# Kernel tuning notes

Hardware: AMD Instinct MI355X
Metric: run time of the kernel (lower is better)

## Reference

```python
import jax, jax.numpy as jnp
import numpy as np

L, E, H, C, N = 3, 512, 8, 64, 65536
DH = E // H
LN_EPS = 1e-5


def setup_inputs() -> dict:
    key = jax.random.key(0)
    ks = jax.random.split(key, 10)
    s = 1.0 / np.sqrt(E)
    return {
        "support_features": jax.random.normal(ks[0], (N, E), jnp.float32),
        "support_labels": jax.random.randint(ks[1], (N,), 0, C),
        "W1": jax.random.normal(ks[2], (L, E, E), jnp.float32) * s,
        "b1": jnp.zeros((L, E), jnp.float32),
        "gamma": jnp.ones((L, E), jnp.float32),
        "beta": jnp.zeros((L, E), jnp.float32),
        "W2": jax.random.normal(ks[3], (L, E, E), jnp.float32) * s,
        "b2": jnp.zeros((L, E), jnp.float32),
        "Wq": jax.random.normal(ks[4], (E, E), jnp.float32) * s,
        "bq": jnp.zeros((E,), jnp.float32),
        "Wk": jax.random.normal(ks[5], (E, E), jnp.float32) * s,
        "bk": jnp.zeros((E,), jnp.float32),
        "Wv": jax.random.normal(ks[6], (E, E), jnp.float32) * s,
        "bv": jnp.zeros((E,), jnp.float32),
        "Wo": jax.random.normal(ks[7], (E, E), jnp.float32) * s,
        "bo": jnp.zeros((E,), jnp.float32),
        "level_weights": jnp.ones((L,), jnp.float32) / L,
        "level_temps": jnp.ones((L,), jnp.float32),
    }


def _layer_norm(x, g, b):
    mu = jnp.mean(x, axis=-1, keepdims=True)
    var = jnp.var(x, axis=-1, keepdims=True)
    return (x - mu) * jax.lax.rsqrt(var + LN_EPS) * g + b


def reference(support_features, support_labels, W1, b1, gamma, beta, W2, b2,
              Wq, bq, Wk, bk, Wv, bv, Wo, bo, level_weights, level_temps):
    # class membership mask [C, N]; segment counts [C]
    onehot = support_labels[None, :] == jnp.arange(C)[:, None]
    counts = jnp.sum(onehot, axis=1).astype(support_features.dtype)
    scale = 1.0 / np.sqrt(DH)
    protos = []
    for l in range(L):  # small fixed number of levels
        # prototype MLP (dropout inactive at eval)
        h = jnp.maximum(_layer_norm(support_features @ W1[l] + b1[l], gamma[l], beta[l]), 0.0)
        feat = h @ W2[l] + b2[l]                              # [N, E]
        # per-class mean context (segment mean) -> query
        ctx = (onehot.astype(feat.dtype) @ feat) / counts[:, None]  # [C, E]
        q = (ctx @ Wq + bq).reshape(C, H, DH)
        k = (feat @ Wk + bk).reshape(N, H, DH)
        v = (feat @ Wv + bv).reshape(N, H, DH)
        scores = jnp.einsum('chd,nhd->chn', q, k) * scale      # [C, H, N]
        scores = jnp.where(onehot[:, None, :], scores, -jnp.inf)
        attn = jax.nn.softmax(scores, axis=-1)
        out = jnp.einsum('chn,nhd->chd', attn, v).reshape(C, E)
        protos.append(out @ Wo + bo)                           # [C, E]
    lw = jax.nn.softmax(level_weights)
    final = protos[0] * (lw[0] / level_temps[0])
    for i in range(1, L):
        final = final + protos[i] * (lw[i] / level_temps[i])
    return final
```

## Files before the change

### kernel.cpp

```cpp
#include <hip/hip_runtime.h>
#include <math.h>

#define N_SUP 65536
#define E_DIM 512
#define H_HEADS 8
#define C_CLS 64
#define DHD 64
#define L_LEV 3
#define LN_EPS 1e-5f
#define ATTN_SPLITS 8
#define CTX_SPLITS 16
#define SCAT_BLOCKS 256
#define KV_LD 1024

typedef _Float16 f16x8 __attribute__((ext_vector_type(8)));
typedef _Float16 f16x4 __attribute__((ext_vector_type(4)));
typedef float f32x4 __attribute__((ext_vector_type(4)));

__device__ __forceinline__ void gload_lds16(const void* g, void* lds) {
    __builtin_amdgcn_global_load_lds((const __attribute__((address_space(1))) void*)g,
                                     (__attribute__((address_space(3))) void*)lds,
                                     16, 0, 0);
}

__global__ __launch_bounds__(256)
void hgemm_bt(const _Float16* __restrict__ A, int lda, size_t aStride,
              const _Float16* __restrict__ Bt, size_t btStride,
              const float* __restrict__ bias, size_t biasStride,
              _Float16* __restrict__ C, int ldc, size_t cStride, int nCol) {
    const int z = blockIdx.y;
    A += z * aStride; Bt += z * btStride; bias += z * biasStride; C += z * cStride;

    const int nRow = gridDim.x / nCol;
    const int R = nRow < 64 ? nRow : 64;
    const int bid = blockIdx.x;
    const int bandSz = R * nCol;
    const int band = bid / bandSz;
    const int rem = bid % bandSz;
    const int colT = rem / R;
    const int rowT = band * R + (rem % R);

    __shared__ _Float16 As[128][32];
    __shared__ _Float16 Bs[128][32];
    const int tid = threadIdx.x;
    const int wave = tid >> 6, lane = tid & 63;
    const int row0 = rowT * 128, col0 = colT * 128;
    const int wm = (wave & 1) * 64, wn = (wave >> 1) * 64;

    const int ci0 = wave * 128 + lane, ci1 = ci0 + 64;
    const int r0 = ci0 >> 2, gc0 = (ci0 & 3) ^ ((r0 >> 1) & 3);
    const int r1 = ci1 >> 2, gc1 = (ci1 & 3) ^ ((r1 >> 1) & 3);
    const _Float16* Ar0 = A + (size_t)(row0 + r0) * lda + gc0 * 8;
    const _Float16* Ar1 = A + (size_t)(row0 + r1) * lda + gc1 * 8;
    const _Float16* Br0 = Bt + (size_t)(col0 + r0) * E_DIM + gc0 * 8;
    const _Float16* Br1 = Bt + (size_t)(col0 + r1) * E_DIM + gc1 * 8;
    char* ldsA = (char*)&As[0][0] + wave * 2048;
    char* ldsB = (char*)&Bs[0][0] + wave * 2048;

    const int m = lane & 15, q = lane >> 4;
    const int koff = ((q ^ ((m >> 1) & 3))) * 8;

    f32x4 acc[4][4];
#pragma unroll
    for (int i = 0; i < 4; ++i)
#pragma unroll
        for (int j = 0; j < 4; ++j) acc[i][j] = (f32x4){0.f, 0.f, 0.f, 0.f};

    for (int k0 = 0; k0 < E_DIM; k0 += 32) {
        gload_lds16(Ar0 + k0, ldsA);
        gload_lds16(Ar1 + k0, ldsA + 1024);
        gload_lds16(Br0 + k0, ldsB);
        gload_lds16(Br1 + k0, ldsB + 1024);
        __syncthreads();

        f16x8 af[4], bf[4];
#pragma unroll
        for (int i = 0; i < 4; ++i)
            af[i] = *(const f16x8*)&As[wm + i * 16 + m][koff];
#pragma unroll
        for (int j = 0; j < 4; ++j)
            bf[j] = *(const f16x8*)&Bs[wn + j * 16 + m][koff];
#pragma unroll
        for (int i = 0; i < 4; ++i)
#pragma unroll
            for (int j = 0; j < 4; ++j)
                acc[i][j] = __builtin_amdgcn_mfma_f32_16x16x32_f16(af[i], bf[j], acc[i][j], 0, 0, 0);
        __syncthreads();
    }

#pragma unroll
    for (int i = 0; i < 4; ++i) {
        const int rbase = row0 + wm + i * 16 + q * 4;
#pragma unroll
        for (int j = 0; j < 4; ++j) {
            const int col = col0 + wn + j * 16 + m;
            const float bv = bias[col];
#pragma unroll
            for (int r = 0; r < 4; ++r)
                C[(size_t)(rbase + r) * ldc + col] = (_Float16)(acc[i][j][r] + bv);
        }
    }
}

__global__ __launch_bounds__(256)
void conv32to16(const float* __restrict__ in, _Float16* __restrict__ out, int n4) {
    int i = blockIdx.x * 256 + threadIdx.x;
    if (i < n4) {
        f32x4 v = ((const f32x4*)in)[i];
        f16x4 o = {(_Float16)v[0], (_Float16)v[1], (_Float16)v[2], (_Float16)v[3]};
        ((f16x4*)out)[i] = o;
    }
}

__global__ __launch_bounds__(256)
void transpose_all(const float* __restrict__ W1, const float* __restrict__ Wk,
                   const float* __restrict__ Wv, const float* __restrict__ Wq,
                   _Float16* __restrict__ W1allT, _Float16* __restrict__ WkvqT) {
    const int z = blockIdx.z;
    const float* src;
    _Float16* dst;
    const size_t MSZ = (size_t)E_DIM * E_DIM;
    if (z < 3)       { src = W1 + z * MSZ; dst = W1allT + z * MSZ; }
    else if (z == 3) { src = Wk;           dst = WkvqT; }
    else if (z == 4) { src = Wv;           dst = WkvqT + MSZ; }
    else             { src = Wq;           dst = WkvqT + 2 * MSZ; }

    __shared__ float t[32][33];
    const int k0 = blockIdx.x * 32, n0 = blockIdx.y * 32;
    const int tx = threadIdx.x & 31, ty = threadIdx.x >> 5;
#pragma unroll
    for (int r = 0; r < 32; r += 8)
        t[ty + r][tx] = src[(size_t)(k0 + ty + r) * E_DIM + n0 + tx];
    __syncthreads();
#pragma unroll
    for (int r = 0; r < 32; r += 8)
        dst[(size_t)(n0 + ty + r) * E_DIM + k0 + tx] = (_Float16)t[tx][ty + r];
}

__global__ __launch_bounds__(256)
void bias_compose(const float* __restrict__ b2, const float* __restrict__ Wk,
                  const float* __restrict__ Wv, const float* __restrict__ Wq,
                  const float* __restrict__ bk, const float* __restrict__ bv,
                  const float* __restrict__ bq, float* __restrict__ bcomp) {
    const int l = blockIdx.y;
    const int n = blockIdx.x * 256 + threadIdx.x;
    const float* W; const float* bb; int nn;
    if (n < 512)       { W = Wk; bb = bk; nn = n; }
    else if (n < 1024) { W = Wv; bb = bv; nn = n - 512; }
    else               { W = Wq; bb = bq; nn = n - 1024; }
    float acc = 0.f;
    for (int j = 0; j < E_DIM; ++j)
        acc = fmaf(b2[l * E_DIM + j], W[(size_t)j * E_DIM + nn], acc);
    bcomp[l * 1536 + n] = acc + bb[nn];
}

__global__ __launch_bounds__(256)
void ln_relu_all(_Float16* __restrict__ P, const float* __restrict__ gamma,
                 const float* __restrict__ beta) {
    const int row = blockIdx.x * 4 + (threadIdx.x >> 6);
    const int l = blockIdx.y;
    const int lane = threadIdx.x & 63;
    _Float16* prow = P + (size_t)row * (L_LEV * E_DIM) + l * E_DIM + lane * 8;
    const float* g = gamma + l * E_DIM + lane * 8;
    const float* b = beta  + l * E_DIM + lane * 8;
    f16x8 v = *(const f16x8*)prow;
    float x[8];
    float s = 0.f, s2 = 0.f;
#pragma unroll
    for (int e = 0; e < 8; ++e) {
        x[e] = (float)v[e];
        s += x[e];
        s2 = fmaf(x[e], x[e], s2);
    }
#pragma unroll
    for (int off = 32; off; off >>= 1) {
        s  += __shfl_xor(s, off);
        s2 += __shfl_xor(s2, off);
    }
    const float mean = s * (1.f / E_DIM);
    const float var  = s2 * (1.f / E_DIM) - mean * mean;
    const float rstd = rsqrtf(var + LN_EPS);
    f32x4 g0 = *(const f32x4*)g;
    f32x4 g1 = *(const f32x4*)(g + 4);
    f32x4 b0 = *(const f32x4*)b;
    f32x4 b1 = *(const f32x4*)(b + 4);
    f16x8 o;
#pragma unroll
    for (int e = 0; e < 4; ++e) {
        o[e]     = (_Float16)fmaxf(fmaf((x[e]     - mean) * rstd, g0[e], b0[e]), 0.f);
        o[e + 4] = (_Float16)fmaxf(fmaf((x[e + 4] - mean) * rstd, g1[e], b1[e]), 0.f);
    }
    *(f16x8*)prow = o;
}

__global__ __launch_bounds__(256)
void label_block_hist(const int* __restrict__ labels, int* __restrict__ blockCounts) {
    __shared__ int h[C_CLS];
    const int tid = threadIdx.x;
    if (tid < C_CLS) h[tid] = 0;
    __syncthreads();
    atomicAdd(&h[labels[blockIdx.x * 256 + tid]], 1);
    __syncthreads();
    if (tid < C_CLS) blockCounts[blockIdx.x * C_CLS + tid] = h[tid];
}

__global__ __launch_bounds__(64)
void scan_offsets(const int* __restrict__ blockCounts, int* __restrict__ counts,
                  int* __restrict__ offs, int* __restrict__ blockOffs) {
    const int c = threadIdx.x;
    int total = 0;
    for (int b = 0; b < SCAT_BLOCKS; ++b) total += blockCounts[b * C_CLS + c];
    counts[c] = total;
    __shared__ int tot[C_CLS];
    tot[c] = total;
    __syncthreads();
    int off = 0;
    for (int cc = 0; cc < c; ++cc) off += tot[cc];
    offs[c] = off;
    if (c == C_CLS - 1) offs[C_CLS] = off + total;
    int run = off;
    for (int b = 0; b < SCAT_BLOCKS; ++b) {
        blockOffs[b * C_CLS + c] = run;
        run += blockCounts[b * C_CLS + c];
    }
}

__global__ __launch_bounds__(256)
void scatter_sorted(const int* __restrict__ labels, const int* __restrict__ blockOffs,
                    int* __restrict__ members) {
    __shared__ int cur[C_CLS];
    const int tid = threadIdx.x;
    if (tid < C_CLS) cur[tid] = blockOffs[blockIdx.x * C_CLS + tid];
    __syncthreads();
    const int i = blockIdx.x * 256 + tid;
    const int c = labels[i];
    const int p = atomicAdd(&cur[c], 1);
    members[p] = i;
}

__global__ __launch_bounds__(256)
void zero_f32(float* __restrict__ p, int n) {
    int i = blockIdx.x * 256 + threadIdx.x;
    if (i < n) p[i] = 0.f;
}

__global__ __launch_bounds__(256)
void ctx_partial(const _Float16* __restrict__ P, const int* __restrict__ members,
                 const int* __restrict__ offsets, float* __restrict__ hpart) {
    const int c = blockIdx.x, split = blockIdx.y, l = blockIdx.z;
    const _Float16* src = P + (size_t)l * E_DIM;
    const int tid = threadIdx.x;
    const int wave = tid >> 6, lane = tid & 63;
    const int start = offsets[c], end = offsets[c + 1];
    const int wg = split * 4 + wave;
    const int stride = 4 * CTX_SPLITS;
    const int ld = L_LEV * E_DIM;

    float acc[8];
#pragma unroll
    for (int e = 0; e < 8; ++e) acc[e] = 0.f;

    int i = start + wg;
    for (; i + stride < end; i += 2 * stride) {
        const int n0 = members[i];
        const int n1 = members[i + stride];
        f16x8 r0 = *(const f16x8*)(src + (size_t)n0 * ld + lane * 8);
        f16x8 r1 = *(const f16x8*)(src + (size_t)n1 * ld + lane * 8);
#pragma unroll
        for (int e = 0; e < 8; ++e) acc[e] += (float)r0[e] + (float)r1[e];
    }
    if (i < end) {
        const int n0 = members[i];
        f16x8 r0 = *(const f16x8*)(src + (size_t)n0 * ld + lane * 8);
#pragma unroll
        for (int e = 0; e < 8; ++e) acc[e] += (float)r0[e];
    }

    __shared__ float red[4][64][8];
#pragma unroll
    for (int e = 0; e < 8; ++e) red[wave][lane][e] = acc[e];
    __syncthreads();
    float* dst = hpart + (((size_t)l * C_CLS + c) * CTX_SPLITS + split) * E_DIM;
#pragma unroll
    for (int t = 0; t < 2; ++t) {
        const int col = tid * 2 + t;
        const int ln = col >> 3, e = col & 7;
        dst[col] = red[0][ln][e] + red[1][ln][e] + red[2][ln][e] + red[3][ln][e];
    }
}

__global__ __launch_bounds__(256)
void row_gemm_q(const float* __restrict__ hpart, const int* __restrict__ counts,
                const _Float16* __restrict__ W2compT, const float* __restrict__ bcomp,
                float* __restrict__ q) {
    const int c = blockIdx.x, l = blockIdx.y;
    const int tid = threadIdx.x;
    const float inv = 1.f / (float)counts[c];
    __shared__ float xrow[E_DIM];
    const float* hp = hpart + ((size_t)l * C_CLS + c) * CTX_SPLITS * E_DIM;
    float s0 = 0.f, s1 = 0.f;
#pragma unroll
    for (int s = 0; s < CTX_SPLITS; ++s) {
        s0 += hp[s * E_DIM + tid];
        s1 += hp[s * E_DIM + tid + 256];
    }
    xrow[tid]       = s0 * inv;
    xrow[tid + 256] = s1 * inv;
    __syncthreads();

    const _Float16* Wq = W2compT + (size_t)l * 1536 * E_DIM + (size_t)1024 * E_DIM;
    const float* bias = bcomp + l * 1536 + 1024;
    const int n0 = tid, n1 = tid + 256;
    float a0 = 0.f, a1 = 0.f;
#pragma unroll 4
    for (int k0 = 0; k0 < E_DIM; k0 += 8) {
        f16x8 w0 = *(const f16x8*)(Wq + (size_t)n0 * E_DIM + k0);
        f16x8 w1 = *(const f16x8*)(Wq + (size_t)n1 * E_DIM + k0);
#pragma unroll
        for (int e = 0; e < 8; ++e) {
            const float xv = xrow[k0 + e];
            a0 = fmaf(xv, (float)w0[e], a0);
            a1 = fmaf(xv, (float)w1[e], a1);
        }
    }
    float* qq = q + (size_t)l * C_CLS * E_DIM;
    qq[c * E_DIM + n0] = a0 + bias[n0];
    qq[c * E_DIM + n1] = a1 + bias[n1];
}

__global__ __launch_bounds__(256)
void attn_partial(const float* __restrict__ q, const _Float16* __restrict__ kv,
                  const int* __restrict__ members, const int* __restrict__ offsets,
                  float* __restrict__ pm, float* __restrict__ pl,
                  float* __restrict__ po) {
    const int c = blockIdx.x, h = blockIdx.y, s = blockIdx.z;
    const int tid = threadIdx.x;
    const int wave = tid >> 6, lane = tid & 63;
    const int start = offsets[c], end = offsets[c + 1];
    const int g = s * 4 + wave;

    float qv[64];
    const bool active = (start + g * 64) < end;
    if (active) {
        const float* qrow = q + c * E_DIM + h * DHD;
#pragma unroll
        for (int d = 0; d < 64; ++d) qv[d] = qrow[d];
    }

    __shared__ float ps[4][64];
    float m = -INFINITY, lsum = 0.f, out = 0.f;

    for (int ch0 = start + g * 64; ch0 < end; ch0 += 4 * ATTN_SPLITS * 64) {
        const int nvalid = min(64, end - ch0);
        const int idx = ch0 + lane;
        const int mi = members[idx < end ? idx : end - 1];
        const _Float16* krow = kv + (size_t)mi * KV_LD + h * DHD;
        float dot = 0.f;
#pragma unroll
        for (int j = 0; j < 8; ++j) {
            f16x8 kr = *(const f16x8*)(krow + j * 8);
#pragma unroll
            for (int e = 0; e < 8; ++e)
                dot = fmaf((float)kr[e], qv[j * 8 + e], dot);
        }
        float sc = (lane < nvalid) ? dot * 0.125f : -INFINITY;
        float cm = sc;
#pragma unroll
        for (int off = 32; off; off >>= 1) cm = fmaxf(cm, __shfl_xor(cm, off));
        const float nm = fmaxf(m, cm);
        const float alpha = __expf(m - nm);
        const float p = (lane < nvalid) ? __expf(sc - nm) : 0.f;
        ps[wave][lane] = p;
        out *= alpha;
        lsum *= alpha;
        m = nm;
        asm volatile("" ::: "memory");
#pragma unroll 16
        for (int j = 0; j < 64; ++j) {
            const int nj = __shfl(mi, j);
            const float pj = ps[wave][j];
            const float vv = (float)kv[(size_t)nj * KV_LD + E_DIM + h * DHD + lane];
            out = fmaf(pj, vv, out);
            lsum += pj;
        }
    }

    __shared__ float rm[4], rl[4], racc[4][64];
    racc[wave][lane] = out;
    if (lane == 0) { rm[wave] = m; rl[wave] = lsum; }
    __syncthreads();
    if (wave == 0) {
        float M = fmaxf(fmaxf(rm[0], rm[1]), fmaxf(rm[2], rm[3]));
        float o = 0.f, Lt = 0.f;
#pragma unroll
        for (int w = 0; w < 4; ++w) {
            const float al = (rm[w] > -INFINITY) ? __expf(rm[w] - M) : 0.f;
            o  += al * racc[w][lane];
            Lt += al * rl[w];
        }
        const int pidx = (c * H_HEADS + h) * ATTN_SPLITS + s;
        po[pidx * 64 + lane] = o;
        if (lane == 0) { pm[pidx] = M; pl[pidx] = Lt; }
    }
}

__global__ __launch_bounds__(256)
void proto_accum(const float* __restrict__ pm, const float* __restrict__ pl,
                 const float* __restrict__ po, const float* __restrict__ Wo,
                 const float* __restrict__ bo, const float* __restrict__ lvlw,
                 const float* __restrict__ lvlt, int l, float* __restrict__ out) {
    const int c = blockIdx.x;
    const int tid = threadIdx.x;
    const int wave = tid >> 6, lane = tid & 63;
    __shared__ float xrow[E_DIM];
#pragma unroll
    for (int hh = wave; hh < H_HEADS; hh += 4) {
        const int ch = c * H_HEADS + hh;
        float M = -INFINITY;
#pragma unroll
        for (int s = 0; s < ATTN_SPLITS; ++s) M = fmaxf(M, pm[ch * ATTN_SPLITS + s]);
        float o = 0.f, Lt = 0.f;
#pragma unroll
        for (int s = 0; s < ATTN_SPLITS; ++s) {
            const int pidx = ch * ATTN_SPLITS + s;
            const float al = (pm[pidx] > -INFINITY) ? __expf(pm[pidx] - M) : 0.f;
            o  += al * po[pidx * 64 + lane];
            Lt += al * pl[pidx];
        }
        xrow[hh * 64 + lane] = o / Lt;
    }
    __syncthreads();

    float a0 = 0.f, a1 = 0.f;
#pragma unroll 8
    for (int k = 0; k < E_DIM; ++k) {
        float cv = xrow[k];
        a0 = fmaf(cv, Wo[(size_t)k * E_DIM + tid], a0);
        a1 = fmaf(cv, Wo[(size_t)k * E_DIM + tid + 256], a1);
    }
    float w0 = lvlw[0], w1 = lvlw[1], w2 = lvlw[2];
    float mx = fmaxf(w0, fmaxf(w1, w2));
    float e0 = expf(w0 - mx), e1 = expf(w1 - mx), e2 = expf(w2 - mx);
    float ssum = e0 + e1 + e2;
    float lw = (l == 0 ? e0 : (l == 1 ? e1 : e2)) / ssum;
    float coef = lw / lvlt[l];
    float r0 = (a0 + bo[tid]) * coef;
    float r1 = (a1 + bo[tid + 256]) * coef;
    if (l == 0) {
        out[c * E_DIM + tid]       = r0;
        out[c * E_DIM + tid + 256] = r1;
    } else {
        out[c * E_DIM + tid]       += r0;
        out[c * E_DIM + tid + 256] += r1;
    }
}

extern "C" void kernel_launch(void* const* d_in, const int* in_sizes, int n_in,
                              void* d_out, int out_size, void* d_ws, size_t ws_size,
                              hipStream_t stream) {
    const float* X      = (const float*)d_in[0];
    const int*   labels = (const int*)  d_in[1];
    const float* W1     = (const float*)d_in[2];
    const float* b1     = (const float*)d_in[3];
    const float* gamma  = (const float*)d_in[4];
    const float* beta   = (const float*)d_in[5];
    const float* W2     = (const float*)d_in[6];
    const float* b2     = (const float*)d_in[7];
    const float* Wq     = (const float*)d_in[8];
    const float* bq     = (const float*)d_in[9];
    const float* Wk     = (const float*)d_in[10];
    const float* bk     = (const float*)d_in[11];
    const float* Wv     = (const float*)d_in[12];
    const float* bv     = (const float*)d_in[13];
    const float* Wo     = (const float*)d_in[14];
    const float* bo     = (const float*)d_in[15];
    const float* lvlw   = (const float*)d_in[16];
    const float* lvlt   = (const float*)d_in[17];
    float* out = (float*)d_out;

    char* p = (char*)d_ws;
    const size_t MSZ = (size_t)E_DIM * E_DIM;
    _Float16* Xh      = (_Float16*)p; p += (size_t)N_SUP * E_DIM * 2;
    _Float16* bufPall = (_Float16*)p; p += (size_t)N_SUP * E_DIM * L_LEV * 2;
    _Float16* bufKV   = (_Float16*)p; p += (size_t)N_SUP * KV_LD * 2;
    _Float16* W1allT  = (_Float16*)p; p += L_LEV * MSZ * 2;
    _Float16* WkvqT   = (_Float16*)p; p += 3 * MSZ * 2;
    _Float16* W2f16   = (_Float16*)p; p += L_LEV * MSZ * 2;
    _Float16* W2compT = (_Float16*)p; p += (size_t)L_LEV * 1536 * E_DIM * 2;
    float* zeros512 = (float*)p; p += E_DIM * sizeof(float);
    float* bcomp = (float*)p; p += L_LEV * 1536 * sizeof(float);
    float* hpart = (float*)p; p += (size_t)L_LEV * C_CLS * CTX_SPLITS * E_DIM * sizeof(float);
    float* qb    = (float*)p; p += (size_t)L_LEV * C_CLS * E_DIM * sizeof(float);
    float* pm    = (float*)p; p += C_CLS * H_HEADS * ATTN_SPLITS * sizeof(float);
    float* pl    = (float*)p; p += C_CLS * H_HEADS * ATTN_SPLITS * sizeof(float);
    float* po    = (float*)p; p += (size_t)C_CLS * H_HEADS * ATTN_SPLITS * 64 * sizeof(float);
    int* counts      = (int*)p; p += 256;
    int* offs        = (int*)p; p += 512;
    int* members     = (int*)p; p += (size_t)N_SUP * sizeof(int);
    int* blockCounts = (int*)p; p += (size_t)SCAT_BLOCKS * C_CLS * sizeof(int);
    int* blockOffs   = (int*)p; p += (size_t)SCAT_BLOCKS * C_CLS * sizeof(int);

    label_block_hist<<<SCAT_BLOCKS, 256, 0, stream>>>(labels, blockCounts);
    scan_offsets<<<1, 64, 0, stream>>>(blockCounts, counts, offs, blockOffs);
    scatter_sorted<<<SCAT_BLOCKS, 256, 0, stream>>>(labels, blockOffs, members);

    conv32to16<<<(N_SUP * E_DIM / 4) / 256, 256, 0, stream>>>(X, Xh, N_SUP * E_DIM / 4);
    conv32to16<<<(int)(L_LEV * MSZ / 4 / 256), 256, 0, stream>>>(W2, W2f16, L_LEV * MSZ / 4);
    transpose_all<<<dim3(16, 16, 6), 256, 0, stream>>>(W1, Wk, Wv, Wq, W1allT, WkvqT);
    zero_f32<<<2, 256, 0, stream>>>(zeros512, E_DIM);

    hgemm_bt<<<dim3(12 * 4, L_LEV), 256, 0, stream>>>(
        WkvqT, E_DIM, 0, W2f16, MSZ, zeros512, 0,
        W2compT, E_DIM, (size_t)1536 * E_DIM, 4);
    bias_compose<<<dim3(6, L_LEV), 256, 0, stream>>>(b2, Wk, Wv, Wq, bk, bv, bq, bcomp);

    const int nRow = N_SUP / 128;
    hgemm_bt<<<dim3(nRow * 12, 1), 256, 0, stream>>>(
        Xh, E_DIM, 0, W1allT, 0, b1, 0, bufPall, L_LEV * E_DIM, 0, 12);
    ln_relu_all<<<dim3(N_SUP / 4, L_LEV), 256, 0, stream>>>(bufPall, gamma, beta);

    ctx_partial<<<dim3(C_CLS, CTX_SPLITS, L_LEV), 256, 0, stream>>>(
        bufPall, members, offs, hpart);
    row_gemm_q<<<dim3(C_CLS, L_LEV), 256, 0, stream>>>(
        hpart, counts, W2compT, bcomp, qb);

    for (int l = 0; l < L_LEV; ++l) {
        hgemm_bt<<<dim3(nRow * 8, 1), 256, 0, stream>>>(
            bufPall + (size_t)l * E_DIM, L_LEV * E_DIM, 0,
            W2compT + (size_t)l * 1536 * E_DIM, 0,
            bcomp + l * 1536, 0, bufKV, KV_LD, 0, 8);
        attn_partial<<<dim3(C_CLS, H_HEADS, ATTN_SPLITS), 256, 0, stream>>>(
            qb + (size_t)l * C_CLS * E_DIM, bufKV, members, offs, pm, pl, po);
        proto_accum<<<C_CLS, 256, 0, stream>>>(pm, pl, po, Wo, bo, lvlw, lvlt, l, out);
    }
}
```

Measured before the change: 1.004 ms.

## Replace 128x128 GEMM with double-buffered 256x256 tile MFMA kernel

Replaces the 128x128x32 single-buffered fp16 GEMM with a 256x256x64 tile kernel using 512 threads, two LDS stages and async global-to-LDS loads for the next stage, issued while MFMAs run under raised wave priority. Larger tiles raise arithmetic intensity and cut redundant global loads. Double buffering with explicit vmcnt waits is meant to hide load latency. The cost is 128 KB of LDS per block and 128 accumulator registers per thread, which may limit occupancy. The small weight-composition GEMM also runs with very few blocks.

Result: slower. 1.038 ms (+3.5%).

```diff
diff --git a/kernel.cpp b/kernel.cpp
--- a/kernel.cpp
+++ b/kernel.cpp
@@ -23,8 +23,8 @@
                                      16, 0, 0);
 }
 
-__global__ __launch_bounds__(256)
-void hgemm_bt(const _Float16* __restrict__ A, int lda, size_t aStride,
+__global__ __launch_bounds__(512, 2)
+void hgemm256(const _Float16* __restrict__ A, int lda, size_t aStride,
               const _Float16* __restrict__ Bt, size_t btStride,
               const float* __restrict__ bias, size_t biasStride,
               _Float16* __restrict__ C, int ldc, size_t cStride, int nCol) {
@@ -39,65 +39,107 @@
     const int rem = bid % bandSz;
     const int colT = rem / R;
     const int rowT = band * R + (rem % R);
-
-    __shared__ _Float16 As[128][32];
-    __shared__ _Float16 Bs[128][32];
+    const int row0 = rowT * 256, col0 = colT * 256;
+
+    __shared__ _Float16 smem[2][2][256][64];
+
     const int tid = threadIdx.x;
     const int wave = tid >> 6, lane = tid & 63;
-    const int row0 = rowT * 128, col0 = colT * 128;
-    const int wm = (wave & 1) * 64, wn = (wave >> 1) * 64;
-
-    const int ci0 = wave * 128 + lane, ci1 = ci0 + 64;
-    const int r0 = ci0 >> 2, gc0 = (ci0 & 3) ^ ((r0 >> 1) & 3);
-    const int r1 = ci1 >> 2, gc1 = (ci1 & 3) ^ ((r1 >> 1) & 3);
-    const _Float16* Ar0 = A + (size_t)(row0 + r0) * lda + gc0 * 8;
-    const _Float16* Ar1 = A + (size_t)(row0 + r1) * lda + gc1 * 8;
-    const _Float16* Br0 = Bt + (size_t)(col0 + r0) * E_DIM + gc0 * 8;
-    const _Float16* Br1 = Bt + (size_t)(col0 + r1) * E_DIM + gc1 * 8;
-    char* ldsA = (char*)&As[0][0] + wave * 2048;
-    char* ldsB = (char*)&Bs[0][0] + wave * 2048;
-
+    const int wm2 = (wave & 1) * 128;
+    const int wn4 = (wave >> 1) * 64;
     const int m = lane & 15, q = lane >> 4;
-    const int koff = ((q ^ ((m >> 1) & 3))) * 8;
-
-    f32x4 acc[4][4];
-#pragma unroll
-    for (int i = 0; i < 4; ++i)
+
+    const int sr = tid >> 3;
+    const int sb = tid & 7;
+    const int sblk = sb ^ (sr & 7);
+
+    const _Float16* Asrc = A + (size_t)(row0 + sr) * lda + sblk * 8;
+    const _Float16* Bsrc = Bt + (size_t)(col0 + sr) * E_DIM + sblk * 8;
+    const size_t aPass = (size_t)64 * lda;
+    const size_t bPass = (size_t)64 * E_DIM;
+
+#define STAGE_TILE(k0, s)                                                     \
+    {                                                                         \
+        char* la = (char*)&smem[s][0][0][0] + wave * 1024;                    \
+        char* lb = (char*)&smem[s][1][0][0] + wave * 1024;                    \
+        _Pragma("unroll")                                                     \
+        for (int p = 0; p < 4; ++p)                                           \
+            gload_lds16(Asrc + (size_t)p * aPass + (k0), la + p * 8192);      \
+        _Pragma("unroll")                                                     \
+        for (int p = 0; p < 4; ++p)                                           \
+            gload_lds16(Bsrc + (size_t)p * bPass + (k0), lb + p * 8192);      \
+    }
+
+    f32x4 acc[8][4];
+#pragma unroll
+    for (int i = 0; i < 8; ++i)
 #pragma unroll
         for (int j = 0; j < 4; ++j) acc[i][j] = (f32x4){0.f, 0.f, 0.f, 0.f};
 
-    for (int k0 = 0; k0 < E_DIM; k0 += 32) {
-        gload_lds16(Ar0 + k0, ldsA);
-        gload_lds16(Ar1 + k0, ldsA + 1024);
-        gload_lds16(Br0 + k0, ldsB);
-        gload_lds16(Br1 + k0, ldsB + 1024);
-        __syncthreads();
-
-        f16x8 af[4], bf[4];
-#pragma unroll
-        for (int i = 0; i < 4; ++i)
-            af[i] = *(const f16x8*)&As[wm + i * 16 + m][koff];
-#pragma unroll
-        for (int j = 0; j < 4; ++j)
-            bf[j] = *(const f16x8*)&Bs[wn + j * 16 + m][koff];
-#pragma unroll
-        for (int i = 0; i < 4; ++i)
-#pragma unroll
-            for (int j = 0; j < 4; ++j)
-                acc[i][j] = __builtin_amdgcn_mfma_f32_16x16x32_f16(af[i], bf[j], acc[i][j], 0, 0, 0);
-        __syncthreads();
-    }
-
-#pragma unroll
-    for (int i = 0; i < 4; ++i) {
-        const int rbase = row0 + wm + i * 16 + q * 4;
-#pragma unroll
-        for (int j = 0; j < 4; ++j) {
-            const int col = col0 + wn + j * 16 + m;
+    const int c0k = ((q) ^ (m & 7)) * 8;
+    const int c1k = ((4 + q) ^ (m & 7)) * 8;
+
+    STAGE_TILE(0, 0);
+    STAGE_TILE(64, 1);
+
+    for (int t = 0; t < 8; ++t) {
+        const int s = t & 1;
+        if (t < 7) {
+            asm volatile("s_waitcnt vmcnt(8)" ::: "memory");
+        } else {
+            asm volatile("s_waitcnt vmcnt(0)" ::: "memory");
+        }
+        __builtin_amdgcn_s_barrier();
+
+        const _Float16* As = &smem[s][0][0][0];
+        const _Float16* Bs = &smem[s][1][0][0];
+
+        f16x8 a0[8], a1[8], b0[4], b1[4];
+#pragma unroll
+        for (int fr = 0; fr < 8; ++fr) {
+            const int rb = (wm2 + fr * 16 + m) * 64;
+            a0[fr] = *(const f16x8*)&As[rb + c0k];
+            a1[fr] = *(const f16x8*)&As[rb + c1k];
+        }
+#pragma unroll
+        for (int fc = 0; fc < 4; ++fc) {
+            const int rb = (wn4 + fc * 16 + m) * 64;
+            b0[fc] = *(const f16x8*)&Bs[rb + c0k];
+            b1[fc] = *(const f16x8*)&Bs[rb + c1k];
+        }
+        asm volatile("s_waitcnt lgkmcnt(0)" ::: "memory");
+        __builtin_amdgcn_s_barrier();
+
+        if (t + 2 < 8) {
+            const int k0n = (t + 2) * 64;
+            STAGE_TILE(k0n, s);
+        }
+
+        __builtin_amdgcn_s_setprio(1);
+#pragma unroll
+        for (int fr = 0; fr < 8; ++fr)
+#pragma unroll
+            for (int fc = 0; fc < 4; ++fc)
+                acc[fr][fc] = __builtin_amdgcn_mfma_f32_16x16x32_f16(a0[fr], b0[fc], acc[fr][fc], 0, 0, 0);
+#pragma unroll
+        for (int fr = 0; fr < 8; ++fr)
+#pragma unroll
+            for (int fc = 0; fc < 4; ++fc)
+                acc[fr][fc] = __builtin_amdgcn_mfma_f32_16x16x32_f16(a1[fr], b1[fc], acc[fr][fc], 0, 0, 0);
+        __builtin_amdgcn_s_setprio(0);
+    }
+#undef STAGE_TILE
+
+#pragma unroll
+    for (int fr = 0; fr < 8; ++fr) {
+        const int rbase = row0 + wm2 + fr * 16 + q * 4;
+#pragma unroll
+        for (int fc = 0; fc < 4; ++fc) {
+            const int col = col0 + wn4 + fc * 16 + m;
             const float bv = bias[col];
 #pragma unroll
             for (int r = 0; r < 4; ++r)
-                C[(size_t)(rbase + r) * ldc + col] = (_Float16)(acc[i][j][r] + bv);
+                C[(size_t)(rbase + r) * ldc + col] = (_Float16)(acc[fr][fc][r] + bv);
         }
     }
 }
@@ -509,14 +551,14 @@
     transpose_all<<<dim3(16, 16, 6), 256, 0, stream>>>(W1, Wk, Wv, Wq, W1allT, WkvqT);
     zero_f32<<<2, 256, 0, stream>>>(zeros512, E_DIM);
 
-    hgemm_bt<<<dim3(12 * 4, L_LEV), 256, 0, stream>>>(
+    hgemm256<<<dim3(6 * 2, L_LEV), 512, 0, stream>>>(
         WkvqT, E_DIM, 0, W2f16, MSZ, zeros512, 0,
-        W2compT, E_DIM, (size_t)1536 * E_DIM, 4);
+        W2compT, E_DIM, (size_t)1536 * E_DIM, 2);
     bias_compose<<<dim3(6, L_LEV), 256, 0, stream>>>(b2, Wk, Wv, Wq, bk, bv, bq, bcomp);
 
-    const int nRow = N_SUP / 128;
-    hgemm_bt<<<dim3(nRow * 12, 1), 256, 0, stream>>>(
-        Xh, E_DIM, 0, W1allT, 0, b1, 0, bufPall, L_LEV * E_DIM, 0, 12);
+    const int nRowT = N_SUP / 256;
+    hgemm256<<<dim3(nRowT * 6, 1), 512, 0, stream>>>(
+        Xh, E_DIM, 0, W1allT, 0, b1, 0, bufPall, L_LEV * E_DIM, 0, 6);
     ln_relu_all<<<dim3(N_SUP / 4, L_LEV), 256, 0, stream>>>(bufPall, gamma, beta);
 
     ctx_partial<<<dim3(C_CLS, CTX_SPLITS, L_LEV), 256, 0, stream>>>(
@@ -525,10 +567,10 @@
         hpart, counts, W2compT, bcomp, qb);
 
     for (int l = 0; l < L_LEV; ++l) {
-        hgemm_bt<<<dim3(nRow * 8, 1), 256, 0, stream>>>(
+        hgemm256<<<dim3(nRowT * 4, 1), 512, 0, stream>>>(
             bufPall + (size_t)l * E_DIM, L_LEV * E_DIM, 0,
             W2compT + (size_t)l * 1536 * E_DIM, 0,
-            bcomp + l * 1536, 0, bufKV, KV_LD, 0, 8);
+            bcomp + l * 1536, 0, bufKV, KV_LD, 0, 4);
         attn_partial<<<dim3(C_CLS, H_HEADS, ATTN_SPLITS), 256, 0, stream>>>(
             qb + (size_t)l * C_CLS * E_DIM, bufKV, members, offs, pm, pl, po);
         proto_accum<<<C_CLS, 256, 0, stream>>>(pm, pl, po, Wo, bo, lvlw, lvlt, l, out);
```
